# Performance work log

Hardware: AMD Instinct MI355X
Metric: run time of the kernel (lower is better)

Reference implementation:

```python
import jax, jax.numpy as jnp
import numpy as np

D_IN = 1024
D_OUT = 1024
NUM_HEADS = 16
HEAD_DIM = D_OUT // NUM_HEADS


def setup_inputs() -> dict:
    key = jax.random.key(0)
    k_x, k_qkv, k_pw, k_pb = jax.random.split(key, 4)
    x = jax.random.normal(k_x, (2, 2048, D_IN), dtype=jnp.float32)
    # torch nn.Linear(d_in, 3*d_out, bias=False): weight [3*d_out, d_in]
    w_qkv = jax.random.normal(k_qkv, (3 * D_OUT, D_IN), dtype=jnp.float32) * (1.0 / np.sqrt(D_IN))
    # proj: nn.Linear(d_out, d_out) with bias
    w_proj = jax.random.normal(k_pw, (D_OUT, D_OUT), dtype=jnp.float32) * (1.0 / np.sqrt(D_OUT))
    b_proj = jax.random.normal(k_pb, (D_OUT,), dtype=jnp.float32) * 0.01
    return {"x": x, "w_qkv": w_qkv, "w_proj": w_proj, "b_proj": b_proj}


def reference(x, w_qkv, w_proj, b_proj):
    B, S, _ = x.shape
    # fused QKV projection: [B,S,3*D_OUT]
    qkv = jnp.einsum('bsd,ed->bse', x, w_qkv)
    qkv = qkv.reshape(B, S, 3, NUM_HEADS, HEAD_DIM)
    q, k, v = jnp.moveaxis(qkv, 2, 0)  # each [B,S,H,Dh]
    scale = 1.0 / jnp.sqrt(jnp.asarray(HEAD_DIM, dtype=x.dtype))
    # scores [B,H,S,S]
    scores = jnp.einsum('bqhd,bkhd->bhqk', q, k) * scale
    causal = jnp.tril(jnp.ones((S, S), dtype=bool))
    scores = jnp.where(causal, scores, jnp.asarray(-jnp.inf, dtype=scores.dtype))
    attn = jax.nn.softmax(scores, axis=-1)
    ctx = jnp.einsum('bhqk,bkhd->bqhd', attn, v)  # [B,S,H,Dh]
    ctx = ctx.reshape(B, S, D_OUT)
    return jnp.einsum('bsd,ed->bse', ctx, w_proj) + b_proj
```

## Files before the change

### kernel.cpp

```cpp
#include <hip/hip_runtime.h>
#include <hip/hip_bf16.h>
#include <cstdint>

#define B_SZ   2
#define S_LEN  2048
#define NH     16
#define LDA    72

using f32x4 = __attribute__((ext_vector_type(4))) float;
typedef __bf16 bf16x8 __attribute__((ext_vector_type(8)));
typedef __bf16 bf16x4 __attribute__((ext_vector_type(4)));

__device__ inline float bf2f(unsigned short u) {
    union { unsigned int i; float f; } v; v.i = ((unsigned int)u) << 16; return v.f;
}
__device__ inline unsigned short f2bf(float f) {
    union { float f; unsigned int i; } v; v.f = f;
    unsigned int r = v.i + 0x7fff + ((v.i >> 16) & 1);
    return (unsigned short)(r >> 16);
}
__device__ inline f32x4 mfma16(bf16x8 a, bf16x8 b, f32x4 c) {
    return __builtin_amdgcn_mfma_f32_16x16x32_bf16(a, b, c, 0, 0, 0);
}
__device__ inline unsigned pack_bf16x2(float lo, float hi) {
    float2 f2; f2.x = lo; f2.y = hi;
    __hip_bfloat162 bb = __float22bfloat162_rn(f2);
    union { __hip_bfloat162 b; unsigned u; } cv; cv.b = bb;
    return cv.u;
}
__device__ inline void ldsbar() {
    __builtin_amdgcn_sched_barrier(0);
    asm volatile("s_waitcnt lgkmcnt(0)" ::: "memory");
    __builtin_amdgcn_s_barrier();
    __builtin_amdgcn_sched_barrier(0);
}
__device__ inline void stC(float* C, size_t idx, float v)  { C[idx] = v; }
__device__ inline void stC(__bf16* C, size_t idx, float v) { ((unsigned short*)C)[idx] = f2bf(v); }

__global__ __launch_bounds__(256) void f2b2_kernel(
    const float* __restrict__ a, int na4, __bf16* __restrict__ outa,
    const float* __restrict__ b, int nb4, __bf16* __restrict__ outb)
{
    int i = blockIdx.x * blockDim.x + threadIdx.x;
    const float* src; __bf16* dst; int idx;
    if (i < na4)           { src = a; dst = outa; idx = i; }
    else if (i < na4 + nb4){ src = b; dst = outb; idx = i - na4; }
    else return;
    float4 v = ((const float4*)src)[idx];
    ushort4 o;
    o.x = f2bf(v.x); o.y = f2bf(v.y); o.z = f2bf(v.z); o.w = f2bf(v.w);
    ((ushort4*)dst)[idx] = o;
}

__global__ __launch_bounds__(256) void f2b_kernel(
    const float* __restrict__ in, __bf16* __restrict__ out, int n4)
{
    int i = blockIdx.x * blockDim.x + threadIdx.x;
    if (i < n4) {
        float4 v = ((const float4*)in)[i];
        ushort4 o;
        o.x = f2bf(v.x); o.y = f2bf(v.y); o.z = f2bf(v.z); o.w = f2bf(v.w);
        ((ushort4*)out)[i] = o;
    }
}

template <typename TO, int HAS_BIAS>
__global__ __launch_bounds__(256) void gemm128(
    const __bf16* __restrict__ A, const __bf16* __restrict__ W,
    const float* __restrict__ bias, TO* __restrict__ C,
    int M, int N, int K)
{
    __shared__ __bf16 Alds[3][128 * 32];
    __shared__ __bf16 Blds[3][128 * 32];
    const int tid  = threadIdx.x, lane = tid & 63, w = tid >> 6;
    const int c16  = lane & 15, quad = lane >> 4;
    const int mBase = blockIdx.y * 128, nBase = blockIdx.x * 128;
    const int moff = (w & 1) * 64, noff = (w >> 1) * 64;

    f32x4 acc[4][4];
#pragma unroll
    for (int i = 0; i < 4; ++i)
#pragma unroll
        for (int j = 0; j < 4; ++j) acc[i][j] = (f32x4){0.f, 0.f, 0.f, 0.f};

    auto stage = [&](int buf, int k0) {
#pragma unroll
        for (int p = 0; p < 2; ++p) {
            const int linear = p * 256 + tid;
            const int row = linear >> 2;
            const int seg = (linear & 3) ^ (row & 3);
            const int lbase = (p * 256 + w * 64) * 8;
            const __bf16* ga = A + (size_t)(mBase + row) * K + k0 + seg * 8;
            const __bf16* gb = W + (size_t)(nBase + row) * K + k0 + seg * 8;
            __builtin_amdgcn_global_load_lds(
                (const __attribute__((address_space(1))) void*)ga,
                (__attribute__((address_space(3))) void*)(&Alds[buf][lbase]), 16, 0, 0);
            __builtin_amdgcn_global_load_lds(
                (const __attribute__((address_space(1))) void*)gb,
                (__attribute__((address_space(3))) void*)(&Blds[buf][lbase]), 16, 0, 0);
        }
    };

    stage(0, 0);
    if (32 < K) stage(1, 32);
    int cur = 0;
    for (int k0 = 0; k0 < K; k0 += 32) {
        __builtin_amdgcn_sched_barrier(0);
        if (k0 + 32 < K) asm volatile("s_waitcnt vmcnt(4) lgkmcnt(0)" ::: "memory");
        else             asm volatile("s_waitcnt vmcnt(0) lgkmcnt(0)" ::: "memory");
        __builtin_amdgcn_s_barrier();
        __builtin_amdgcn_sched_barrier(0);

        if (k0 + 64 < K) stage(cur == 0 ? 2 : cur - 1, k0 + 64);

        bf16x8 af[4], bw[4];
#pragma unroll
        for (int i = 0; i < 4; ++i) {
            const int rowA = moff + i * 16 + c16;
            af[i] = *(const bf16x8*)&Alds[cur][rowA * 32 + ((quad ^ (rowA & 3)) << 3)];
            const int rowB = noff + i * 16 + c16;
            bw[i] = *(const bf16x8*)&Blds[cur][rowB * 32 + ((quad ^ (rowB & 3)) << 3)];
        }
#pragma unroll
        for (int i = 0; i < 4; ++i)
#pragma unroll
            for (int j = 0; j < 4; ++j)
                acc[i][j] = mfma16(af[i], bw[j], acc[i][j]);
        cur = (cur == 2) ? 0 : cur + 1;
    }

#pragma unroll
    for (int j = 0; j < 4; ++j) {
        const int col = nBase + noff + j * 16 + c16;
        const float bv = HAS_BIAS ? bias[col] : 0.f;
#pragma unroll
        for (int i = 0; i < 4; ++i)
#pragma unroll
            for (int r = 0; r < 4; ++r) {
                const int row = mBase + moff + i * 16 + quad * 4 + r;
                stC(C, (size_t)row * N + col, acc[i][j][r] + bv);
            }
    }
}

template <typename TO, int HAS_BIAS>
__global__ __launch_bounds__(256) void gemm64(
    const __bf16* __restrict__ A, const __bf16* __restrict__ W,
    const float* __restrict__ bias, TO* __restrict__ C,
    int M, int N, int K)
{
    __shared__ __bf16 Alds[3][64 * 32];
    __shared__ __bf16 Blds[3][128 * 32];
    const int tid  = threadIdx.x, lane = tid & 63, w = tid >> 6;
    const int c16  = lane & 15, quad = lane >> 4;
    const int mBase = blockIdx.y * 64, nBase = blockIdx.x * 128;
    const int moff = (w & 1) * 32, noff = (w >> 1) * 64;

    f32x4 acc[2][4];
#pragma unroll
    for (int i = 0; i < 2; ++i)
#pragma unroll
        for (int j = 0; j < 4; ++j) acc[i][j] = (f32x4){0.f, 0.f, 0.f, 0.f};

    auto stage = [&](int buf, int k0) {
        {
            const int row = tid >> 2;
            const int seg = (tid & 3) ^ (row & 3);
            const int lbase = (w * 64) * 8;
            const __bf16* ga = A + (size_t)(mBase + row) * K + k0 + seg * 8;
            __builtin_amdgcn_global_load_lds(
                (const __attribute__((address_space(1))) void*)ga,
                (__attribute__((address_space(3))) void*)(&Alds[buf][lbase]), 16, 0, 0);
        }
#pragma unroll
        for (int p = 0; p < 2; ++p) {
            const int linear = p * 256 + tid;
            const int row = linear >> 2;
            const int seg = (linear & 3) ^ (row & 3);
            const int lbase = (p * 256 + w * 64) * 8;
            const __bf16* gb = W + (size_t)(nBase + row) * K + k0 + seg * 8;
            __builtin_amdgcn_global_load_lds(
                (const __attribute__((address_space(1))) void*)gb,
                (__attribute__((address_space(3))) void*)(&Blds[buf][lbase]), 16, 0, 0);
        }
    };

    stage(0, 0);
    if (32 < K) stage(1, 32);
    int cur = 0;
    for (int k0 = 0; k0 < K; k0 += 32) {
        __builtin_amdgcn_sched_barrier(0);
        if (k0 + 32 < K) asm volatile("s_waitcnt vmcnt(3) lgkmcnt(0)" ::: "memory");
        else             asm volatile("s_waitcnt vmcnt(0) lgkmcnt(0)" ::: "memory");
        __builtin_amdgcn_s_barrier();
        __builtin_amdgcn_sched_barrier(0);

        if (k0 + 64 < K) stage(cur == 0 ? 2 : cur - 1, k0 + 64);

        bf16x8 af[2], bw[4];
#pragma unroll
        for (int i = 0; i < 2; ++i) {
            const int rowA = moff + i * 16 + c16;
            af[i] = *(const bf16x8*)&Alds[cur][rowA * 32 + ((quad ^ (rowA & 3)) << 3)];
        }
#pragma unroll
        for (int j = 0; j < 4; ++j) {
            const int rowB = noff + j * 16 + c16;
            bw[j] = *(const bf16x8*)&Blds[cur][rowB * 32 + ((quad ^ (rowB & 3)) << 3)];
        }
#pragma unroll
        for (int i = 0; i < 2; ++i)
#pragma unroll
            for (int j = 0; j < 4; ++j)
                acc[i][j] = mfma16(af[i], bw[j], acc[i][j]);
        cur = (cur == 2) ? 0 : cur + 1;
    }

#pragma unroll
    for (int j = 0; j < 4; ++j) {
        const int col = nBase + noff + j * 16 + c16;
        const float bv = HAS_BIAS ? bias[col] : 0.f;
#pragma unroll
        for (int i = 0; i < 2; ++i)
#pragma unroll
            for (int r = 0; r < 4; ++r) {
                const int row = mBase + moff + i * 16 + quad * 4 + r;
                stC(C, (size_t)row * N + col, acc[i][j][r] + bv);
            }
    }
}

__global__ __launch_bounds__(256) void attn(
    const __bf16* __restrict__ qkv, __bf16* __restrict__ ctx)
{
    __shared__ __bf16 Qs[64 * LDA];
    __shared__ __bf16 Ks[64 * LDA];
    __shared__ __bf16 Vs[64 * LDA];

    const int tid  = threadIdx.x;
    const int lane = tid & 63;
    const int w    = tid >> 6;
    const int c16  = lane & 15;
    const int quad = lane >> 4;
    const int bh = blockIdx.x, b = bh >> 4, h = bh & 15;
    const int y  = blockIdx.y;

    const int a  = y & 7, uq = y >> 3;
    const int qt = (uq == 0) ? (31 - a) : (uq == 1) ? (16 + a)
                 : (uq == 2) ? (15 - a) : a;
    const int c1 = qt + 1;
    const int qBase = qt * 64;

    const float QS = 0.125f * 1.4426950408889634f;

    const int krow0 = tid >> 3;
    const int kd0   = (tid & 7) * 8;
    const int u     = tid & 31;
    const int dblk  = tid >> 5;
    const int vcol  = 32 * (u & 1) + 8 * ((u >> 1) & 3) + 2 * (u >> 3);

    const size_t rowB = (size_t)b * S_LEN;

    const __bf16* kp0 = qkv + (rowB + krow0) * 3072 + 1024 + h * 64 + kd0;
    const __bf16* kp1 = kp0 + (size_t)32 * 3072;
    const __bf16* vp0 = qkv + (rowB + 2 * u) * 3072 + 2048 + h * 64 + dblk * 8;
    const __bf16* vp1 = vp0 + (size_t)3072;

    uint4 kr0 = *(const uint4*)kp0;
    uint4 kr1 = *(const uint4*)kp1;
    uint4 vr0 = *(const uint4*)vp0;
    uint4 vr1 = *(const uint4*)vp1;

#pragma unroll
    for (int p = 0; p < 2; ++p) {
        const int linear = p * 256 + tid;
        const int row = linear >> 3;
        const int d0 = (linear & 7) * 8;
        const __bf16* g = qkv + (rowB + qBase + row) * 3072 + h * 64 + d0;
        uint4 raw = *(const uint4*)g;
        const unsigned short* uu = (const unsigned short*)&raw;
        unsigned short tmp[8];
#pragma unroll
        for (int jj = 0; jj < 8; ++jj) tmp[jj] = f2bf(bf2f(uu[jj]) * QS);
        *(uint4*)&Qs[row * LDA + d0] = *(const uint4*)tmp;
    }
    ldsbar();

    const bf16x8 aq0 = *(const bf16x8*)&Qs[(w * 16 + c16) * LDA + quad * 8];
    const bf16x8 aq1 = *(const bf16x8*)&Qs[(w * 16 + c16) * LDA + 32 + quad * 8];

    float lp = 0.f;
    f32x4 acc_o[4];
#pragma unroll
    for (int j = 0; j < 4; ++j) acc_o[j] = (f32x4){0.f, 0.f, 0.f, 0.f};

    for (int cc = 0; cc < c1; ++cc) {
        *(uint4*)&Ks[krow0 * LDA + kd0]        = kr0;
        *(uint4*)&Ks[(krow0 + 32) * LDA + kd0] = kr1;
        {
            const unsigned short* e1 = (const unsigned short*)&vr0;
            const unsigned short* e2 = (const unsigned short*)&vr1;
#pragma unroll
            for (int d = 0; d < 8; ++d) {
                const unsigned pack = (unsigned)e1[d] | ((unsigned)e2[d] << 16);
                *(unsigned*)&Vs[(dblk * 8 + d) * LDA + vcol] = pack;
            }
        }
        ldsbar();

        if (cc + 1 < c1) {
            kp0 += (size_t)64 * 3072; kp1 += (size_t)64 * 3072;
            vp0 += (size_t)64 * 3072; vp1 += (size_t)64 * 3072;
            kr0 = *(const uint4*)kp0;
            kr1 = *(const uint4*)kp1;
            vr0 = *(const uint4*)vp0;
            vr1 = *(const uint4*)vp1;
        }

        f32x4 sc[4];
#pragma unroll
        for (int j = 0; j < 4; ++j) sc[j] = (f32x4){0.f, 0.f, 0.f, 0.f};
#pragma unroll
        for (int j = 0; j < 4; ++j) {
            bf16x8 bk0 = *(const bf16x8*)&Ks[(j * 16 + c16) * LDA + quad * 8];
            bf16x8 bk1 = *(const bf16x8*)&Ks[(j * 16 + c16) * LDA + 32 + quad * 8];
            sc[j] = mfma16(bk0, aq0, sc[j]);
            sc[j] = mfma16(bk1, aq1, sc[j]);
        }

        if (cc == qt) {
            const int q = qBase + w * 16 + c16;
#pragma unroll
            for (int j = 0; j < 4; ++j) {
#pragma unroll
                for (int r = 0; r < 4; ++r) {
                    const int key = cc * 64 + j * 16 + quad * 4 + r;
                    if (key > q) sc[j][r] = -1e30f;
                }
            }
        }

        float p_[4][4];
#pragma unroll
        for (int j = 0; j < 4; ++j)
#pragma unroll
            for (int r = 0; r < 4; ++r)
                p_[j][r] = exp2f(sc[j][r]);
#pragma unroll
        for (int j = 0; j < 4; ++j)
            lp += (p_[j][0] + p_[j][1]) + (p_[j][2] + p_[j][3]);

        union { unsigned uu[4]; bf16x8 v; } B0, B1;
#pragma unroll
        for (int j = 0; j < 4; ++j) {
            B0.uu[j] = pack_bf16x2(p_[j][0], p_[j][1]);
            B1.uu[j] = pack_bf16x2(p_[j][2], p_[j][3]);
        }
        const bf16x8 bp0 = B0.v;
        const bf16x8 bp1 = B1.v;

#pragma unroll
        for (int jd = 0; jd < 4; ++jd) {
            bf16x8 av0 = *(const bf16x8*)&Vs[(jd * 16 + c16) * LDA + quad * 8];
            bf16x8 av1 = *(const bf16x8*)&Vs[(jd * 16 + c16) * LDA + 32 + quad * 8];
            acc_o[jd] = mfma16(av0, bp0, acc_o[jd]);
            acc_o[jd] = mfma16(av1, bp1, acc_o[jd]);
        }
        ldsbar();
    }

    lp += __shfl_xor(lp, 16);
    lp += __shfl_xor(lp, 32);

    const float inv = 1.0f / lp;
    const size_t rowO = (rowB + qBase + w * 16 + c16) * 1024 + h * 64;
#pragma unroll
    for (int jd = 0; jd < 4; ++jd) {
        bf16x4 ov;
#pragma unroll
        for (int r = 0; r < 4; ++r) ov[r] = (__bf16)(acc_o[jd][r] * inv);
        *(bf16x4*)&ctx[rowO + jd * 16 + quad * 4] = ov;
    }
}

extern "C" void kernel_launch(void* const* d_in, const int* in_sizes, int n_in,
                              void* d_out, int out_size, void* d_ws, size_t ws_size,
                              hipStream_t stream) {
    const float* x      = (const float*)d_in[0];
    const float* w_qkv  = (const float*)d_in[1];
    const float* w_proj = (const float*)d_in[2];
    const float* b_proj = (const float*)d_in[3];
    float* out = (float*)d_out;

    __bf16* qkvb = (__bf16*)d_ws;
    __bf16* xb   = qkvb + (size_t)4096 * 3072;
    __bf16* wqb  = xb + (size_t)4096 * 1024;
    __bf16* ctxb = xb;
    __bf16* wpb  = wqb;

    const int M = B_SZ * S_LEN;
    const int nx4 = 4096 * 1024 / 4, nq4 = 3072 * 1024 / 4, np4 = 1024 * 1024 / 4;

    f2b2_kernel<<<(nx4 + nq4 + 255) / 256, 256, 0, stream>>>(x, nx4, xb, w_qkv, nq4, wqb);

    gemm128<__bf16, 0><<<dim3(3072 / 128, M / 128), 256, 0, stream>>>(
        xb, wqb, nullptr, qkvb, M, 3072, 1024);

    f2b_kernel<<<(np4 + 255) / 256, 256, 0, stream>>>(w_proj, wpb, np4);

    attn<<<dim3(B_SZ * NH, 32), 256, 0, stream>>>(qkvb, ctxb);

    gemm64<float, 1><<<dim3(1024 / 128, M / 64), 256, 0, stream>>>(
        ctxb, wpb, b_proj, out, M, 1024, 1024);
}
```

Before: 177.7 us.

## Split causal attention KV range across segments and fold Q scaling into GEMM

Each causal query tile is split into 1 to 4 KV segments according to its length, so the attention grid has more, more evenly sized blocks. Segments that are split write unnormalised fp32 partial outputs and row sums to workspace. A new combine kernel sums these partials and normalises them into the bf16 context. The softmax scale for Q is applied in the QKV GEMM epilogue, so attention loads Q fragments straight from global memory instead of staging them through LDS. The trade-off is an extra kernel launch and extra fp32 partial traffic to global memory.

Result: slower. 195.3 us (+9.9%).

```diff
diff --git a/kernel.cpp b/kernel.cpp
--- a/kernel.cpp
+++ b/kernel.cpp
@@ -6,6 +6,7 @@
 #define S_LEN  2048
 #define NH     16
 #define LDA    72
+#define SEGS_PER_BH 80
 
 using f32x4 = __attribute__((ext_vector_type(4))) float;
 typedef __bf16 bf16x8 __attribute__((ext_vector_type(8)));
@@ -36,6 +37,8 @@
 }
 __device__ inline void stC(float* C, size_t idx, float v)  { C[idx] = v; }
 __device__ inline void stC(__bf16* C, size_t idx, float v) { ((unsigned short*)C)[idx] = f2bf(v); }
+
+#define QSF (0.125f * 1.4426950408889634f)
 
 __global__ __launch_bounds__(256) void f2b2_kernel(
     const float* __restrict__ a, int na4, __bf16* __restrict__ outa,
@@ -64,7 +67,7 @@
     }
 }
 
-template <typename TO, int HAS_BIAS>
+template <typename TO, int HAS_BIAS, int QSCALE>
 __global__ __launch_bounds__(256) void gemm128(
     const __bf16* __restrict__ A, const __bf16* __restrict__ W,
     const float* __restrict__ bias, TO* __restrict__ C,
@@ -131,14 +134,16 @@
 
 #pragma unroll
     for (int j = 0; j < 4; ++j) {
-        const int col = nBase + noff + j * 16 + c16;
+        const int colBase = nBase + noff + j * 16;
+        const float qs = (QSCALE && colBase < 1024) ? QSF : 1.0f;
+        const int col = colBase + c16;
         const float bv = HAS_BIAS ? bias[col] : 0.f;
 #pragma unroll
         for (int i = 0; i < 4; ++i)
 #pragma unroll
             for (int r = 0; r < 4; ++r) {
                 const int row = mBase + moff + i * 16 + quad * 4 + r;
-                stC(C, (size_t)row * N + col, acc[i][j][r] + bv);
+                stC(C, (size_t)row * N + col, acc[i][j][r] * qs + bv);
             }
     }
 }
@@ -231,9 +236,9 @@
 }
 
 __global__ __launch_bounds__(256) void attn(
-    const __bf16* __restrict__ qkv, __bf16* __restrict__ ctx)
-{
-    __shared__ __bf16 Qs[64 * LDA];
+    const __bf16* __restrict__ qkv, __bf16* __restrict__ ctx,
+    float* __restrict__ opart, float* __restrict__ lpart)
+{
     __shared__ __bf16 Ks[64 * LDA];
     __shared__ __bf16 Vs[64 * LDA];
 
@@ -245,13 +250,18 @@
     const int bh = blockIdx.x, b = bh >> 4, h = bh & 15;
     const int y  = blockIdx.y;
 
-    const int a  = y & 7, uq = y >> 3;
-    const int qt = (uq == 0) ? (31 - a) : (uq == 1) ? (16 + a)
-                 : (uq == 2) ? (15 - a) : a;
-    const int c1 = qt + 1;
+    int qt, s, k;
+    if (y < 8)       { qt = y;                 s = 0;            k = 1; }
+    else if (y < 24) { qt = 8 + ((y - 8) >> 1);  s = (y - 8) & 1;  k = 2; }
+    else if (y < 48) { int t = y - 24; int q3 = t / 3; qt = 16 + q3; s = t - 3 * q3; k = 3; }
+    else             { int t = y - 48; qt = 24 + (t >> 2); s = t & 3; k = 4; }
+    const int n    = qt + 1;
+    const int base = s * (n / k) + (s < (n % k) ? s : (n % k));
+    const int len  = n / k + (s < (n % k) ? 1 : 0);
+    const int c0 = base, c1 = base + len;
+    const bool split = (k > 1);
+    const int segIdx = bh * SEGS_PER_BH + y;
     const int qBase = qt * 64;
-
-    const float QS = 0.125f * 1.4426950408889634f;
 
     const int krow0 = tid >> 3;
     const int kd0   = (tid & 7) * 8;
@@ -261,9 +271,9 @@
 
     const size_t rowB = (size_t)b * S_LEN;
 
-    const __bf16* kp0 = qkv + (rowB + krow0) * 3072 + 1024 + h * 64 + kd0;
+    const __bf16* kp0 = qkv + (rowB + c0 * 64 + krow0) * 3072 + 1024 + h * 64 + kd0;
     const __bf16* kp1 = kp0 + (size_t)32 * 3072;
-    const __bf16* vp0 = qkv + (rowB + 2 * u) * 3072 + 2048 + h * 64 + dblk * 8;
+    const __bf16* vp0 = qkv + (rowB + c0 * 64 + 2 * u) * 3072 + 2048 + h * 64 + dblk * 8;
     const __bf16* vp1 = vp0 + (size_t)3072;
 
     uint4 kr0 = *(const uint4*)kp0;
@@ -271,30 +281,16 @@
     uint4 vr0 = *(const uint4*)vp0;
     uint4 vr1 = *(const uint4*)vp1;
 
-#pragma unroll
-    for (int p = 0; p < 2; ++p) {
-        const int linear = p * 256 + tid;
-        const int row = linear >> 3;
-        const int d0 = (linear & 7) * 8;
-        const __bf16* g = qkv + (rowB + qBase + row) * 3072 + h * 64 + d0;
-        uint4 raw = *(const uint4*)g;
-        const unsigned short* uu = (const unsigned short*)&raw;
-        unsigned short tmp[8];
-#pragma unroll
-        for (int jj = 0; jj < 8; ++jj) tmp[jj] = f2bf(bf2f(uu[jj]) * QS);
-        *(uint4*)&Qs[row * LDA + d0] = *(const uint4*)tmp;
-    }
-    ldsbar();
-
-    const bf16x8 aq0 = *(const bf16x8*)&Qs[(w * 16 + c16) * LDA + quad * 8];
-    const bf16x8 aq1 = *(const bf16x8*)&Qs[(w * 16 + c16) * LDA + 32 + quad * 8];
+    const __bf16* qp = qkv + (rowB + qBase + w * 16 + c16) * 3072 + h * 64;
+    const bf16x8 aq0 = *(const bf16x8*)(qp + quad * 8);
+    const bf16x8 aq1 = *(const bf16x8*)(qp + 32 + quad * 8);
 
     float lp = 0.f;
     f32x4 acc_o[4];
 #pragma unroll
     for (int j = 0; j < 4; ++j) acc_o[j] = (f32x4){0.f, 0.f, 0.f, 0.f};
 
-    for (int cc = 0; cc < c1; ++cc) {
+    for (int cc = c0; cc < c1; ++cc) {
         *(uint4*)&Ks[krow0 * LDA + kd0]        = kr0;
         *(uint4*)&Ks[(krow0 + 32) * LDA + kd0] = kr1;
         {
@@ -372,15 +368,63 @@
     lp += __shfl_xor(lp, 16);
     lp += __shfl_xor(lp, 32);
 
-    const float inv = 1.0f / lp;
-    const size_t rowO = (rowB + qBase + w * 16 + c16) * 1024 + h * 64;
-#pragma unroll
-    for (int jd = 0; jd < 4; ++jd) {
-        bf16x4 ov;
-#pragma unroll
-        for (int r = 0; r < 4; ++r) ov[r] = (__bf16)(acc_o[jd][r] * inv);
-        *(bf16x4*)&ctx[rowO + jd * 16 + quad * 4] = ov;
-    }
+    if (!split) {
+        const float inv = 1.0f / lp;
+        const size_t rowO = (rowB + qBase + w * 16 + c16) * 1024 + h * 64;
+#pragma unroll
+        for (int jd = 0; jd < 4; ++jd) {
+            bf16x4 ov;
+#pragma unroll
+            for (int r = 0; r < 4; ++r) ov[r] = (__bf16)(acc_o[jd][r] * inv);
+            *(bf16x4*)&ctx[rowO + jd * 16 + quad * 4] = ov;
+        }
+    } else {
+        float* ob = opart + (size_t)segIdx * 4096 + (w * 16 + c16) * 64;
+        if (quad == 0) lpart[segIdx * 64 + w * 16 + c16] = lp;
+#pragma unroll
+        for (int jd = 0; jd < 4; ++jd)
+            *(f32x4*)&ob[jd * 16 + quad * 4] = acc_o[jd];
+    }
+}
+
+__global__ __launch_bounds__(256) void attn_combine(
+    const float* __restrict__ opart, const float* __restrict__ lpart,
+    __bf16* __restrict__ ctx)
+{
+    const int blk = blockIdx.x;
+    const int bh = blk / 24, t = blk - bh * 24;
+    const int qt = 8 + t;
+    const int b = bh >> 4, h = bh & 15;
+    const int k  = (qt < 16) ? 2 : (qt < 24) ? 3 : 4;
+    const int y0 = (qt < 16) ? (2 * qt - 8) : (qt < 24) ? (3 * qt - 24) : (4 * qt - 48);
+    const int segBase = bh * SEGS_PER_BH + y0;
+
+    const int tid = threadIdx.x;
+    const int q  = tid >> 2;
+    const int d0 = (tid & 3) * 16;
+
+    float l = 0.f;
+    for (int s_ = 0; s_ < k; ++s_) l += lpart[(segBase + s_) * 64 + q];
+    const float inv = 1.0f / l;
+
+    float acc[16];
+#pragma unroll
+    for (int i = 0; i < 16; ++i) acc[i] = 0.f;
+    for (int s_ = 0; s_ < k; ++s_) {
+        const float* o = opart + (size_t)(segBase + s_) * 4096 + q * 64 + d0;
+#pragma unroll
+        for (int i = 0; i < 4; ++i) {
+            float4 v = ((const float4*)o)[i];
+            acc[4 * i + 0] += v.x; acc[4 * i + 1] += v.y;
+            acc[4 * i + 2] += v.z; acc[4 * i + 3] += v.w;
+        }
+    }
+    unsigned short outv[16];
+#pragma unroll
+    for (int i = 0; i < 16; ++i) outv[i] = f2bf(acc[i] * inv);
+    __bf16* dst = ctx + ((size_t)(b * S_LEN + qt * 64 + q)) * 1024 + h * 64 + d0;
+    *(uint4*)dst       = *(const uint4*)&outv[0];
+    *(uint4*)(dst + 8) = *(const uint4*)&outv[8];
 }
 
 extern "C" void kernel_launch(void* const* d_in, const int* in_sizes, int n_in,
@@ -397,18 +441,21 @@
     __bf16* wqb  = xb + (size_t)4096 * 1024;
     __bf16* ctxb = xb;
     __bf16* wpb  = wqb;
+    float*  opart = (float*)(wqb + (size_t)3072 * 1024);
+    float*  lpart = opart + (size_t)2560 * 4096;
 
     const int M = B_SZ * S_LEN;
     const int nx4 = 4096 * 1024 / 4, nq4 = 3072 * 1024 / 4, np4 = 1024 * 1024 / 4;
 
     f2b2_kernel<<<(nx4 + nq4 + 255) / 256, 256, 0, stream>>>(x, nx4, xb, w_qkv, nq4, wqb);
 
-    gemm128<__bf16, 0><<<dim3(3072 / 128, M / 128), 256, 0, stream>>>(
+    gemm128<__bf16, 0, 1><<<dim3(3072 / 128, M / 128), 256, 0, stream>>>(
         xb, wqb, nullptr, qkvb, M, 3072, 1024);
 
     f2b_kernel<<<(np4 + 255) / 256, 256, 0, stream>>>(w_proj, wpb, np4);
 
-    attn<<<dim3(B_SZ * NH, 32), 256, 0, stream>>>(qkvb, ctxb);
+    attn<<<dim3(B_SZ * NH, SEGS_PER_BH), 256, 0, stream>>>(qkvb, ctxb, opart, lpart);
+    attn_combine<<<B_SZ * NH * 24, 256, 0, stream>>>(opart, lpart, ctxb);
 
     gemm64<float, 1><<<dim3(1024 / 128, M / 64), 256, 0, stream>>>(
         ctxb, wpb, b_proj, out, M, 1024, 1024);
```

## Double-buffer K/V in attention, fold Q scaling into QKV GEMM, merge conversions

Applied to the files above, without the earlier changes.

The attention kernel now double-buffers K and V in LDS. The next tile is staged while the current one is computed, which removes one barrier per iteration. Q is loaded straight from global memory into registers because the softmax scale is now applied in the QKV GEMM epilogue for the Q columns. The w_proj conversion is merged into the single fp32-to-bf16 conversion launch, so it gets its own workspace region and one kernel launch goes away. The cost is more LDS per block, which may lower occupancy, and Q is rounded to bf16 once after scaling, which changes rounding slightly.

Measured after the change: 179.8 us. About the same (+1.2%).

```diff
diff --git a/kernel.cpp b/kernel.cpp
--- a/kernel.cpp
+++ b/kernel.cpp
@@ -37,14 +37,18 @@
 __device__ inline void stC(float* C, size_t idx, float v)  { C[idx] = v; }
 __device__ inline void stC(__bf16* C, size_t idx, float v) { ((unsigned short*)C)[idx] = f2bf(v); }
 
-__global__ __launch_bounds__(256) void f2b2_kernel(
+#define QSF (0.125f * 1.4426950408889634f)
+
+__global__ __launch_bounds__(256) void f2b3_kernel(
     const float* __restrict__ a, int na4, __bf16* __restrict__ outa,
-    const float* __restrict__ b, int nb4, __bf16* __restrict__ outb)
+    const float* __restrict__ b, int nb4, __bf16* __restrict__ outb,
+    const float* __restrict__ c, int nc4, __bf16* __restrict__ outc)
 {
     int i = blockIdx.x * blockDim.x + threadIdx.x;
     const float* src; __bf16* dst; int idx;
-    if (i < na4)           { src = a; dst = outa; idx = i; }
-    else if (i < na4 + nb4){ src = b; dst = outb; idx = i - na4; }
+    if (i < na4)                  { src = a; dst = outa; idx = i; }
+    else if (i < na4 + nb4)       { src = b; dst = outb; idx = i - na4; }
+    else if (i < na4 + nb4 + nc4) { src = c; dst = outc; idx = i - na4 - nb4; }
     else return;
     float4 v = ((const float4*)src)[idx];
     ushort4 o;
@@ -52,19 +56,7 @@
     ((ushort4*)dst)[idx] = o;
 }
 
-__global__ __launch_bounds__(256) void f2b_kernel(
-    const float* __restrict__ in, __bf16* __restrict__ out, int n4)
-{
-    int i = blockIdx.x * blockDim.x + threadIdx.x;
-    if (i < n4) {
-        float4 v = ((const float4*)in)[i];
-        ushort4 o;
-        o.x = f2bf(v.x); o.y = f2bf(v.y); o.z = f2bf(v.z); o.w = f2bf(v.w);
-        ((ushort4*)out)[i] = o;
-    }
-}
-
-template <typename TO, int HAS_BIAS>
+template <typename TO, int HAS_BIAS, int QSCALE>
 __global__ __launch_bounds__(256) void gemm128(
     const __bf16* __restrict__ A, const __bf16* __restrict__ W,
     const float* __restrict__ bias, TO* __restrict__ C,
@@ -131,14 +123,16 @@
 
 #pragma unroll
     for (int j = 0; j < 4; ++j) {
-        const int col = nBase + noff + j * 16 + c16;
+        const int colBase = nBase + noff + j * 16;
+        const float qs = (QSCALE && colBase < 1024) ? QSF : 1.0f;
+        const int col = colBase + c16;
         const float bv = HAS_BIAS ? bias[col] : 0.f;
 #pragma unroll
         for (int i = 0; i < 4; ++i)
 #pragma unroll
             for (int r = 0; r < 4; ++r) {
                 const int row = mBase + moff + i * 16 + quad * 4 + r;
-                stC(C, (size_t)row * N + col, acc[i][j][r] + bv);
+                stC(C, (size_t)row * N + col, acc[i][j][r] * qs + bv);
             }
     }
 }
@@ -233,9 +227,8 @@
 __global__ __launch_bounds__(256) void attn(
     const __bf16* __restrict__ qkv, __bf16* __restrict__ ctx)
 {
-    __shared__ __bf16 Qs[64 * LDA];
-    __shared__ __bf16 Ks[64 * LDA];
-    __shared__ __bf16 Vs[64 * LDA];
+    __shared__ __bf16 Ks[2][64 * LDA];
+    __shared__ __bf16 Vs[2][64 * LDA];
 
     const int tid  = threadIdx.x;
     const int lane = tid & 63;
@@ -251,8 +244,6 @@
     const int c1 = qt + 1;
     const int qBase = qt * 64;
 
-    const float QS = 0.125f * 1.4426950408889634f;
-
     const int krow0 = tid >> 3;
     const int kd0   = (tid & 7) * 8;
     const int u     = tid & 31;
@@ -271,23 +262,33 @@
     uint4 vr0 = *(const uint4*)vp0;
     uint4 vr1 = *(const uint4*)vp1;
 
-#pragma unroll
-    for (int p = 0; p < 2; ++p) {
-        const int linear = p * 256 + tid;
-        const int row = linear >> 3;
-        const int d0 = (linear & 7) * 8;
-        const __bf16* g = qkv + (rowB + qBase + row) * 3072 + h * 64 + d0;
-        uint4 raw = *(const uint4*)g;
-        const unsigned short* uu = (const unsigned short*)&raw;
-        unsigned short tmp[8];
-#pragma unroll
-        for (int jj = 0; jj < 8; ++jj) tmp[jj] = f2bf(bf2f(uu[jj]) * QS);
-        *(uint4*)&Qs[row * LDA + d0] = *(const uint4*)tmp;
-    }
+    const __bf16* qp = qkv + (rowB + qBase + w * 16 + c16) * 3072 + h * 64;
+    const bf16x8 aq0 = *(const bf16x8*)(qp + quad * 8);
+    const bf16x8 aq1 = *(const bf16x8*)(qp + 32 + quad * 8);
+
+    auto stageKV = [&](int buf) {
+        *(uint4*)&Ks[buf][krow0 * LDA + kd0]        = kr0;
+        *(uint4*)&Ks[buf][(krow0 + 32) * LDA + kd0] = kr1;
+        const unsigned short* e1 = (const unsigned short*)&vr0;
+        const unsigned short* e2 = (const unsigned short*)&vr1;
+#pragma unroll
+        for (int d = 0; d < 8; ++d) {
+            const unsigned pack = (unsigned)e1[d] | ((unsigned)e2[d] << 16);
+            *(unsigned*)&Vs[buf][(dblk * 8 + d) * LDA + vcol] = pack;
+        }
+    };
+    auto loadNext = [&]() {
+        kp0 += (size_t)64 * 3072; kp1 += (size_t)64 * 3072;
+        vp0 += (size_t)64 * 3072; vp1 += (size_t)64 * 3072;
+        kr0 = *(const uint4*)kp0;
+        kr1 = *(const uint4*)kp1;
+        vr0 = *(const uint4*)vp0;
+        vr1 = *(const uint4*)vp1;
+    };
+
+    stageKV(0);
+    if (1 < c1) loadNext();
     ldsbar();
-
-    const bf16x8 aq0 = *(const bf16x8*)&Qs[(w * 16 + c16) * LDA + quad * 8];
-    const bf16x8 aq1 = *(const bf16x8*)&Qs[(w * 16 + c16) * LDA + 32 + quad * 8];
 
     float lp = 0.f;
     f32x4 acc_o[4];
@@ -295,26 +296,10 @@
     for (int j = 0; j < 4; ++j) acc_o[j] = (f32x4){0.f, 0.f, 0.f, 0.f};
 
     for (int cc = 0; cc < c1; ++cc) {
-        *(uint4*)&Ks[krow0 * LDA + kd0]        = kr0;
-        *(uint4*)&Ks[(krow0 + 32) * LDA + kd0] = kr1;
-        {
-            const unsigned short* e1 = (const unsigned short*)&vr0;
-            const unsigned short* e2 = (const unsigned short*)&vr1;
-#pragma unroll
-            for (int d = 0; d < 8; ++d) {
-                const unsigned pack = (unsigned)e1[d] | ((unsigned)e2[d] << 16);
-                *(unsigned*)&Vs[(dblk * 8 + d) * LDA + vcol] = pack;
-            }
-        }
-        ldsbar();
-
+        const int cur = cc & 1;
         if (cc + 1 < c1) {
-            kp0 += (size_t)64 * 3072; kp1 += (size_t)64 * 3072;
-            vp0 += (size_t)64 * 3072; vp1 += (size_t)64 * 3072;
-            kr0 = *(const uint4*)kp0;
-            kr1 = *(const uint4*)kp1;
-            vr0 = *(const uint4*)vp0;
-            vr1 = *(const uint4*)vp1;
+            stageKV(cur ^ 1);
+            if (cc + 2 < c1) loadNext();
         }
 
         f32x4 sc[4];
@@ -322,8 +307,8 @@
         for (int j = 0; j < 4; ++j) sc[j] = (f32x4){0.f, 0.f, 0.f, 0.f};
 #pragma unroll
         for (int j = 0; j < 4; ++j) {
-            bf16x8 bk0 = *(const bf16x8*)&Ks[(j * 16 + c16) * LDA + quad * 8];
-            bf16x8 bk1 = *(const bf16x8*)&Ks[(j * 16 + c16) * LDA + 32 + quad * 8];
+            bf16x8 bk0 = *(const bf16x8*)&Ks[cur][(j * 16 + c16) * LDA + quad * 8];
+            bf16x8 bk1 = *(const bf16x8*)&Ks[cur][(j * 16 + c16) * LDA + 32 + quad * 8];
             sc[j] = mfma16(bk0, aq0, sc[j]);
             sc[j] = mfma16(bk1, aq1, sc[j]);
         }
@@ -361,8 +346,8 @@
 
 #pragma unroll
         for (int jd = 0; jd < 4; ++jd) {
-            bf16x8 av0 = *(const bf16x8*)&Vs[(jd * 16 + c16) * LDA + quad * 8];
-            bf16x8 av1 = *(const bf16x8*)&Vs[(jd * 16 + c16) * LDA + 32 + quad * 8];
+            bf16x8 av0 = *(const bf16x8*)&Vs[cur][(jd * 16 + c16) * LDA + quad * 8];
+            bf16x8 av1 = *(const bf16x8*)&Vs[cur][(jd * 16 + c16) * LDA + 32 + quad * 8];
             acc_o[jd] = mfma16(av0, bp0, acc_o[jd]);
             acc_o[jd] = mfma16(av1, bp1, acc_o[jd]);
         }
@@ -395,18 +380,17 @@
     __bf16* qkvb = (__bf16*)d_ws;
     __bf16* xb   = qkvb + (size_t)4096 * 3072;
     __bf16* wqb  = xb + (size_t)4096 * 1024;
+    __bf16* wpb  = wqb + (size_t)3072 * 1024;
     __bf16* ctxb = xb;
-    __bf16* wpb  = wqb;
 
     const int M = B_SZ * S_LEN;
     const int nx4 = 4096 * 1024 / 4, nq4 = 3072 * 1024 / 4, np4 = 1024 * 1024 / 4;
 
-    f2b2_kernel<<<(nx4 + nq4 + 255) / 256, 256, 0, stream>>>(x, nx4, xb, w_qkv, nq4, wqb);
-
-    gemm128<__bf16, 0><<<dim3(3072 / 128, M / 128), 256, 0, stream>>>(
+    f2b3_kernel<<<(nx4 + nq4 + np4 + 255) / 256, 256, 0, stream>>>(
+        x, nx4, xb, w_qkv, nq4, wqb, w_proj, np4, wpb);
+
+    gemm128<__bf16, 0, 1><<<dim3(3072 / 128, M / 128), 256, 0, stream>>>(
         xb, wqb, nullptr, qkvb, M, 3072, 1024);
-
-    f2b_kernel<<<(np4 + 255) / 256, 256, 0, stream>>>(w_proj, wpb, np4);
 
     attn<<<dim3(B_SZ * NH, 32), 256, 0, stream>>>(qkvb, ctxb);
 
```
